# Performance work log

Measured on AMD Instinct MI355X. Metric: run time of the kernel, lower is better.

The kernel has to match this reference:

```python
import jax, jax.numpy as jnp
import numpy as np

N = 50000
E = 400000
T = 7
FEAT = 7
H = 64
OUT = 4
LN_EPS = 1e-5


def _w(key, shape, scale=0.1):
    return jax.random.normal(key, shape, jnp.float32) * scale


def setup_inputs() -> dict:
    key = jax.random.key(0)
    ks = list(jax.random.split(key, 16))
    p = {}
    p['x'] = jax.random.normal(ks[0], (N, T, FEAT), jnp.float32)
    p['edge_index'] = jax.random.randint(ks[1], (2, E), 0, N)
    p['edge_weight'] = jax.random.uniform(ks[2], (E,), jnp.float32)
    p['Wg1'] = _w(ks[3], (FEAT, H)); p['bg1'] = jnp.zeros((H,), jnp.float32)
    p['Wg2'] = _w(ks[4], (H, H));    p['bg2'] = jnp.zeros((H,), jnp.float32)
    p['ln_g'] = jnp.ones((H,), jnp.float32); p['ln_b'] = jnp.zeros((H,), jnp.float32)
    p['Wih0'] = _w(ks[5], (4 * H, H)); p['Whh0'] = _w(ks[6], (4 * H, H))
    p['bih0'] = jnp.zeros((4 * H,), jnp.float32); p['bhh0'] = jnp.zeros((4 * H,), jnp.float32)
    p['Wih1'] = _w(ks[7], (4 * H, H)); p['Whh1'] = _w(ks[8], (4 * H, H))
    p['bih1'] = jnp.zeros((4 * H,), jnp.float32); p['bhh1'] = jnp.zeros((4 * H,), jnp.float32)
    p['Wm1'] = _w(ks[9], (H, H // 2));  p['bm1'] = jnp.zeros((H // 2,), jnp.float32)
    p['Wm2'] = _w(ks[10], (H // 2, OUT)); p['bm2'] = jnp.zeros((OUT,), jnp.float32)
    p['Wd1'] = _w(ks[11], (H, H // 4)); p['bd1'] = jnp.zeros((H // 4,), jnp.float32)
    p['Wd2'] = _w(ks[12], (H // 4, OUT)); p['bd2'] = jnp.zeros((OUT,), jnp.float32)
    return p


def gcn_norm(edge_index, edge_weight, n):
    # PyG GCNConv default: add self-loops (weight 1), symmetric normalization
    loop = jnp.arange(n)
    src = jnp.concatenate([edge_index[0], loop])
    dst = jnp.concatenate([edge_index[1], loop])
    w = jnp.concatenate([edge_weight, jnp.ones((n,), edge_weight.dtype)])
    deg = jax.ops.segment_sum(w, dst, num_segments=n)
    dinv = jnp.where(deg > 0, jax.lax.rsqrt(deg), 0.0)
    return src, dst, dinv[src] * w * dinv[dst]


def gcn(h, W, b, src, dst, norm, n):
    h = h @ W                          # [N, H] linear transform first
    m = h[src] * norm[:, None]         # gather + edge scaling  [E', H]
    return jax.ops.segment_sum(m, dst, num_segments=n) + b


def layer_norm(h, g, b):
    mu = jnp.mean(h, -1, keepdims=True)
    v = jnp.mean((h - mu) ** 2, -1, keepdims=True)
    return (h - mu) * jax.lax.rsqrt(v + LN_EPS) * g + b


def lstm_layer(xs, Wih, Whh, bih, bhh):
    # xs: [N, T, H]; torch gate order i, f, g, o
    n = xs.shape[0]
    h0 = jnp.zeros((n, Whh.shape[1]), xs.dtype)
    def step(carry, xt):
        h, c = carry
        gates = xt @ Wih.T + h @ Whh.T + bih + bhh
        i, f, g, o = jnp.split(gates, 4, axis=-1)
        c = jax.nn.sigmoid(f) * c + jax.nn.sigmoid(i) * jnp.tanh(g)
        h = jax.nn.sigmoid(o) * jnp.tanh(c)
        return (h, c), h
    _, hs = jax.lax.scan(step, (h0, h0), jnp.swapaxes(xs, 0, 1))
    return jnp.swapaxes(hs, 0, 1)


def reference(x, edge_index, edge_weight, Wg1, bg1, Wg2, bg2, ln_g, ln_b,
              Wih0, Whh0, bih0, bhh0, Wih1, Whh1, bih1, bhh1,
              Wm1, bm1, Wm2, bm2, Wd1, bd1, Wd2, bd2):
    n = x.shape[0]
    src, dst, norm = gcn_norm(edge_index, edge_weight, n)
    outs = []
    for t in range(x.shape[1]):  # fixed small T=7 (lookback)
        h = gcn(x[:, t, :], Wg1, bg1, src, dst, norm, n)
        h = jax.nn.leaky_relu(h, 0.01)
        # dropout is identity in eval mode
        h = gcn(h, Wg2, bg2, src, dst, norm, n)
        h = jax.nn.leaky_relu(h, 0.01)
        h = layer_norm(h, ln_g, ln_b)
        outs.append(h)
    seq = jnp.stack(outs, axis=1)  # [N, T, H]
    seq = lstm_layer(seq, Wih0, Whh0, bih0, bhh0)
    seq = lstm_layer(seq, Wih1, Whh1, bih1, bhh1)
    f = seq[:, -1, :]
    magnitude = jax.nn.relu(jax.nn.leaky_relu(f @ Wm1 + bm1, 0.01) @ Wm2 + bm2) + 1e-4
    direction = jax.nn.relu(f @ Wd1 + bd1) @ Wd2 + bd2
    return (magnitude, direction)
```

## Files before the change

kernel.cpp:

```cpp
#include <hip/hip_runtime.h>
#include <stdint.h>

#define NN 50000
#define NP 50048
#define EE 400000
#define TT 7
#define LN_EPS 1e-5f
#define SIG_SC (-1.4426950408889634f)
#define TANH_SC (2.8853900817779268f)

typedef __attribute__((ext_vector_type(8))) short bf16x8;
typedef __attribute__((ext_vector_type(4))) float f32x4;

__device__ __forceinline__ float leaky01(float x){ return x > 0.f ? x : 0.01f*x; }
__device__ __forceinline__ float fastrcp(float x){ return __builtin_amdgcn_rcpf(x); }
__device__ __forceinline__ float exp2fast(float x){ return __builtin_amdgcn_exp2f(x); }
__device__ __forceinline__ unsigned bf16rne(float f){
  unsigned u = __float_as_uint(f);
  return (u + 0x7fffu + ((u>>16)&1u)) >> 16;
}
__device__ __forceinline__ float bfu(unsigned u){ return __uint_as_float(u<<16); }
__device__ __forceinline__ float bfhi(unsigned u){ return __uint_as_float(u & 0xffff0000u); }

__global__ __launch_bounds__(256) void k_prep_all(
    const float* __restrict__ Wih0, const float* __restrict__ Whh0,
    const float* __restrict__ Wih1, const float* __restrict__ Whh1,
    const float* __restrict__ Wg2,
    const float* __restrict__ bih0, const float* __restrict__ bhh0,
    const float* __restrict__ bih1, const float* __restrict__ bhh1,
    const float* __restrict__ Wm1, const float* __restrict__ Wd1,
    const float* __restrict__ x,
    uint4* __restrict__ WF, uint4* __restrict__ WG2F, uint4* __restrict__ WHF,
    float* __restrict__ BS,
    ushort* __restrict__ xb, float* __restrict__ deg, int* __restrict__ counts){
  int b = blockIdx.x, tid = threadIdx.x;
  if (b < 32){
    int idx = b*256 + tid;
    int L = idx >> 12;
    int r = idx & 4095;
    int lane = r & 63;
    int e = r >> 6;
    int which = e & 1;
    int cs = e >> 1;
    int s = cs & 1, ct = cs >> 1;
    int row = ct*16 + (lane & 15);
    float sc = ((row >> 6) == 2) ? TANH_SC : SIG_SC;
    int kb = s*32 + (lane >> 4)*8;
    const float* W = L ? (which ? Whh1 : Wih1) : (which ? Whh0 : Wih0);
    const float* p = W + row*64 + kb;
    uint4 v;
    v.x = bf16rne(sc*p[0]) | (bf16rne(sc*p[1])<<16);
    v.y = bf16rne(sc*p[2]) | (bf16rne(sc*p[3])<<16);
    v.z = bf16rne(sc*p[4]) | (bf16rne(sc*p[5])<<16);
    v.w = bf16rne(sc*p[6]) | (bf16rne(sc*p[7])<<16);
    WF[idx] = v;
  } else if (b < 34){
    int idx = (b-32)*256 + tid;
    int lane = idx & 63, e = idx >> 6;
    int s = e & 1, ct = e >> 1;
    int kb = s*32 + (lane>>4)*8;
    int c = ct*16 + (lane&15);
    uint4 v;
    v.x = bf16rne(Wg2[(kb+0)*64+c]) | (bf16rne(Wg2[(kb+1)*64+c])<<16);
    v.y = bf16rne(Wg2[(kb+2)*64+c]) | (bf16rne(Wg2[(kb+3)*64+c])<<16);
    v.z = bf16rne(Wg2[(kb+4)*64+c]) | (bf16rne(Wg2[(kb+5)*64+c])<<16);
    v.w = bf16rne(Wg2[(kb+6)*64+c]) | (bf16rne(Wg2[(kb+7)*64+c])<<16);
    WG2F[idx] = v;
  } else if (b < 36){
    int L = b - 34;
    float sc = ((tid >> 6) == 2) ? TANH_SC : SIG_SC;
    BS[L*256+tid] = sc * (L ? (bih1[tid]+bhh1[tid]) : (bih0[tid]+bhh0[tid]));
  } else if (b < 38){
    int idx = (b-36)*256 + tid;
    if (idx < 384){
      int lane = idx & 63, e = idx >> 6;
      int s = e & 1, ct = e >> 1;
      int kb = s*32 + (lane>>4)*8;
      int c = ct*16 + (lane&15);
      float w[8];
      #pragma unroll
      for (int j = 0; j < 8; ++j)
        w[j] = (c < 32) ? Wm1[(kb+j)*32 + c] : Wd1[(kb+j)*16 + (c-32)];
      uint4 v;
      v.x = bf16rne(w[0]) | (bf16rne(w[1])<<16);
      v.y = bf16rne(w[2]) | (bf16rne(w[3])<<16);
      v.z = bf16rne(w[4]) | (bf16rne(w[5])<<16);
      v.w = bf16rne(w[6]) | (bf16rne(w[7])<<16);
      WHF[idx] = v;
    }
  } else if (b < 234){
    int i = (b-38)*256 + tid;
    if (i < NN){ deg[i] = 1.0f; counts[i] = 0; }
  } else {
    int i = (b-234)*256 + tid;
    if (i < NN*49) xb[i] = (ushort)bf16rne(x[i]);
  }
}

__global__ void k_edge_count(const int* __restrict__ src, const int* __restrict__ dst,
                             const float* __restrict__ ew, float* deg, int* counts){
  int e = blockIdx.x*blockDim.x + threadIdx.x;
  if (e < EE){
    int d = dst[e];
    atomicAdd(&deg[d], ew[e]);
    atomicAdd(&counts[d], 1);
  }
}
__global__ __launch_bounds__(256) void k_scan_blk(const int* __restrict__ counts,
                                                  int* locincl, int* bsum, float* deg){
  int tid = threadIdx.x; int i = blockIdx.x*256 + tid;
  if (i < NN) deg[i] = rsqrtf(deg[i]);
  int v = (i < NN) ? counts[i] : 0;
  int lane = tid & 63;
  int val = v;
  #pragma unroll
  for (int off = 1; off < 64; off <<= 1){
    int u = __shfl_up(val, off, 64);
    if (lane >= off) val += u;
  }
  __shared__ int wsum[4];
  if (lane == 63) wsum[tid>>6] = val;
  __syncthreads();
  int w = tid >> 6, pre = 0;
  #pragma unroll
  for (int k = 0; k < 4; ++k) if (k < w) pre += wsum[k];
  int incl = val + pre;
  if (i < NN) locincl[i] = incl;
  if (tid == 255) bsum[blockIdx.x] = incl;
}
__global__ __launch_bounds__(256) void k_scan_top(const int* __restrict__ bsum, int* boff){
  int tid = threadIdx.x;
  int v = (tid < 196) ? bsum[tid] : 0;
  int lane = tid & 63;
  int val = v;
  #pragma unroll
  for (int off = 1; off < 64; off <<= 1){
    int u = __shfl_up(val, off, 64);
    if (lane >= off) val += u;
  }
  __shared__ int wsum[4];
  if (lane == 63) wsum[tid>>6] = val;
  __syncthreads();
  int w = tid >> 6, pre = 0;
  #pragma unroll
  for (int k = 0; k < 4; ++k) if (k < w) pre += wsum[k];
  if (tid < 196) boff[tid] = val + pre - v;
}
__global__ __launch_bounds__(256) void k_scan_fix(const int* __restrict__ locincl,
        const int* __restrict__ boff, const int* __restrict__ counts,
        int* rowptr, int* cursor){
  int i = blockIdx.x*256 + threadIdx.x;
  if (i < NN){
    int r = locincl[i] + boff[blockIdx.x];
    rowptr[i+1] = r;
    cursor[i] = r - counts[i];
  }
  if (i == 0) rowptr[0] = 0;
}
__global__ void k_scatter(const int* __restrict__ src, const int* __restrict__ dst,
                          const float* __restrict__ ew, const float* __restrict__ dinv,
                          int* cursor, uint2* e2){
  int e = blockIdx.x*blockDim.x + threadIdx.x;
  if (e < EE){
    int s = src[e], d = dst[e];
    float nv = dinv[s]*ew[e]*dinv[d];
    int slot = atomicAdd(&cursor[d], 1);
    e2[slot] = make_uint2((uint)s, __float_as_uint(nv));
  }
}

__global__ __launch_bounds__(256) void k_agg_x(const ushort* __restrict__ xb,
        const float* __restrict__ dinv, const int* __restrict__ rowptr,
        const uint2* __restrict__ e2, float* __restrict__ AX){
  int lane = threadIdx.x & 63, w = threadIdx.x >> 6;
  int i = blockIdx.x*4 + w;
  int beg = rowptr[i], end = rowptr[i+1];
  float di = dinv[i];
  float acc = 0.f;
  if (lane < 49) acc = di*di*bfu(xb[(size_t)i*49 + lane]);
  for (int s = beg; s < end; ++s){
    uint2 e = e2[s];
    int cs = (int)e.x; float wv = __uint_as_float(e.y);
    if (lane < 49) acc += wv * bfu(xb[(size_t)cs*49 + lane]);
  }
  if (lane < 49) AX[(size_t)i*49 + lane] = acc;
}
__global__ __launch_bounds__(256) void k_gcn2_mfma(const float* __restrict__ AX,
        const float* __restrict__ Wg1, const float* __restrict__ bg1,
        const uint4* __restrict__ WG2F, ushort* __restrict__ Z2p){
  __shared__ float sw1[448];
  __shared__ float sb1[64];
  __shared__ float sax[8*56];
  __shared__ __align__(16) ushort srb[64*68];
  int tid = threadIdx.x;
  int lane = tid & 63, w = tid >> 6;
  bf16x8 bw[4][2];
  #pragma unroll
  for (int ct = 0; ct < 4; ++ct)
    #pragma unroll
    for (int s = 0; s < 2; ++s){
      uint4 v = WG2F[(ct*2+s)*64 + lane];
      bw[ct][s] = *(bf16x8*)&v;
    }
  for (int i = tid; i < 448; i += 256) sw1[i] = Wg1[i];
  if (tid < 64) sb1[tid] = bg1[tid];
  int nbase = blockIdx.x*8;
  for (int i = tid; i < 448; i += 256){
    int n = i/56, c = i%56;
    sax[i] = (c < 49) ? AX[(size_t)(nbase+n)*49 + c] : 0.f;
  }
  __syncthreads();
  {
    int node = lane >> 3, t = lane & 7;
    float a[7];
    #pragma unroll
    for (int kk = 0; kk < 7; ++kk) a[kk] = sax[node*56 + t*7 + kk];
    ushort hv[16];
    #pragma unroll
    for (int j = 0; j < 16; ++j){
      int k = w*16 + j;
      float acc = sb1[k];
      #pragma unroll
      for (int kk = 0; kk < 7; ++kk) acc += a[kk]*sw1[kk*64+k];
      hv[j] = (ushort)bf16rne(leaky01(acc));
    }
    uint2* dst = (uint2*)&srb[lane*68 + w*16];
    #pragma unroll
    for (int q = 0; q < 4; ++q){
      uint2 v;
      v.x = (uint)hv[q*4+0] | ((uint)hv[q*4+1]<<16);
      v.y = (uint)hv[q*4+2] | ((uint)hv[q*4+3]<<16);
      dst[q] = v;
    }
  }
  __syncthreads();
  int col = lane & 15, quad = lane >> 4;
  bf16x8 afr[2];
  #pragma unroll
  for (int s = 0; s < 2; ++s){
    const ushort* pr = &srb[(w*16 + col)*68 + s*32 + quad*8];
    uint2 lo = *(const uint2*)pr;
    uint2 hi = *(const uint2*)(pr + 4);
    union { uint u[4]; bf16x8 b; } cv;
    cv.u[0]=lo.x; cv.u[1]=lo.y; cv.u[2]=hi.x; cv.u[3]=hi.y;
    afr[s] = cv.b;
  }
  f32x4 acc[4];
  #pragma unroll
  for (int ct = 0; ct < 4; ++ct) acc[ct] = (f32x4){0.f,0.f,0.f,0.f};
  #pragma unroll
  for (int ct = 0; ct < 4; ++ct)
    #pragma unroll
    for (int s = 0; s < 2; ++s)
      acc[ct] = __builtin_amdgcn_mfma_f32_16x16x32_bf16(afr[s], bw[ct][s], acc[ct], 0,0,0);
  int node = nbase + w*2 + (quad>>1);
  #pragma unroll
  for (int ct = 0; ct < 4; ++ct){
    uint2 v;
    v.x = bf16rne(acc[ct][0]) | (bf16rne(acc[ct][1])<<16);
    v.y = bf16rne(acc[ct][2]) | (bf16rne(acc[ct][3])<<16);
    size_t o = ((size_t)node*64 + ct*16 + col)*8 + (quad&1)*4;
    *(uint2*)(Z2p + o) = v;
  }
}
__global__ __launch_bounds__(256) void k_agg_ln_all(const ushort* __restrict__ Z2p,
        const float* __restrict__ dinv, const int* __restrict__ rowptr,
        const uint2* __restrict__ e2,
        const float* __restrict__ bg2, const float* __restrict__ lng,
        const float* __restrict__ lnb, ushort* __restrict__ XT){
  int lane = threadIdx.x & 63, w = threadIdx.x >> 6;
  int i = blockIdx.x*4 + w;
  int beg = rowptr[i], end = rowptr[i+1];
  float di = dinv[i];
  float swt = di*di;
  const uint4* zp = (const uint4*)Z2p;
  float acc[7];
  {
    uint4 v = zp[(size_t)i*64 + lane];
    acc[0] = swt*bfu(v.x); acc[1] = swt*bfhi(v.x);
    acc[2] = swt*bfu(v.y); acc[3] = swt*bfhi(v.y);
    acc[4] = swt*bfu(v.z); acc[5] = swt*bfhi(v.z);
    acc[6] = swt*bfu(v.w);
  }
  for (int s = beg; s < end; ++s){
    uint2 e = e2[s];
    int cs = (int)e.x; float wv = __uint_as_float(e.y);
    uint4 v = zp[(size_t)cs*64 + lane];
    acc[0] = fmaf(wv, bfu(v.x),  acc[0]);
    acc[1] = fmaf(wv, bfhi(v.x), acc[1]);
    acc[2] = fmaf(wv, bfu(v.y),  acc[2]);
    acc[3] = fmaf(wv, bfhi(v.y), acc[3]);
    acc[4] = fmaf(wv, bfu(v.z),  acc[4]);
    acc[5] = fmaf(wv, bfhi(v.z), acc[5]);
    acc[6] = fmaf(wv, bfu(v.w),  acc[6]);
  }
  float b2 = bg2[lane], gl = lng[lane], bl = lnb[lane];
  #pragma unroll
  for (int t = 0; t < 7; ++t){
    float a = leaky01(acc[t] + b2);
    float sum = a;
    #pragma unroll
    for (int off = 32; off >= 1; off >>= 1) sum += __shfl_xor(sum, off, 64);
    float mu = sum * (1.f/64.f);
    float d = a - mu;
    float vs = d*d;
    #pragma unroll
    for (int off = 32; off >= 1; off >>= 1) vs += __shfl_xor(vs, off, 64);
    float rs = rsqrtf(vs*(1.f/64.f) + LN_EPS);
    XT[(size_t)t*NP*64 + (size_t)i*64 + lane] = (ushort)bf16rne(d*rs*gl + bl);
  }
}

__global__ __launch_bounds__(256) void k_lstm_heads(const ushort* __restrict__ xin,
        const uint4* __restrict__ WF, const float* __restrict__ BS,
        const uint4* __restrict__ WHF,
        const float* __restrict__ bm1, const float* __restrict__ bd1,
        const float* __restrict__ Wm2, const float* __restrict__ bm2,
        const float* __restrict__ Wd2, const float* __restrict__ bd2,
        float* __restrict__ out){
  __shared__ __align__(16) ushort XL[7][16][72];
  int tid = threadIdx.x;
  int lane = tid & 63, cp = tid >> 6;
  int base = blockIdx.x*16;
  int col = lane & 15, quad = lane >> 4;
  bf16x8 hfr[2];
  hfr[0] = (bf16x8){0,0,0,0,0,0,0,0};
  hfr[1] = (bf16x8){0,0,0,0,0,0,0,0};

  for (int L = 0; L < 2; ++L){
    bf16x8 bwi[4][2], bwh[4][2];
    const uint4* wf = WF + L*4096;
    #pragma unroll
    for (int g = 0; g < 4; ++g){
      int ct = cp + 4*g;
      #pragma unroll
      for (int s = 0; s < 2; ++s){
        uint4 wi = wf[((ct*2+s)*2+0)*64 + lane];
        uint4 wh = wf[((ct*2+s)*2+1)*64 + lane];
        bwi[g][s] = *(bf16x8*)&wi;
        bwh[g][s] = *(bf16x8*)&wh;
      }
    }
    float bias[4];
    #pragma unroll
    for (int g = 0; g < 4; ++g) bias[g] = BS[L*256 + (cp + 4*g)*16 + col];
    f32x4 cst = (f32x4){0.f,0.f,0.f,0.f};
    if (L){
      hfr[0] = (bf16x8){0,0,0,0,0,0,0,0};
      hfr[1] = (bf16x8){0,0,0,0,0,0,0,0};
    }

    for (int t = 0; t < 7; ++t){
      bf16x8 ax[2];
      if (L == 0){
        #pragma unroll
        for (int s = 0; s < 2; ++s)
          ax[s] = *(const bf16x8*)(xin + (size_t)t*NP*64
                          + (size_t)(base + col)*64 + s*32 + quad*8);
      } else {
        #pragma unroll
        for (int s = 0; s < 2; ++s)
          ax[s] = *(const bf16x8*)&XL[t][col][s*32 + quad*8];
      }
      f32x4 acc[4];
      #pragma unroll
      for (int g = 0; g < 4; ++g){
        float b = bias[g];
        acc[g] = (f32x4){b,b,b,b};
      }
      #pragma unroll
      for (int g = 0; g < 4; ++g){
        #pragma unroll
        for (int s = 0; s < 2; ++s){
          acc[g] = __builtin_amdgcn_mfma_f32_16x16x32_bf16(ax[s], bwi[g][s], acc[g], 0,0,0);
          acc[g] = __builtin_amdgcn_mfma_f32_16x16x32_bf16(hfr[s], bwh[g][s], acc[g], 0,0,0);
        }
      }
      if (L) __syncthreads();
      #pragma unroll
      for (int r = 0; r < 4; ++r){
        float ig = fastrcp(1.f + exp2fast(acc[0][r]));
        float fg = fastrcp(1.f + exp2fast(acc[1][r]));
        float gg = fmaf(-2.f, fastrcp(1.f + exp2fast(acc[2][r])), 1.f);
        float og = fastrcp(1.f + exp2fast(acc[3][r]));
        float cn = fmaf(fg, cst[r], ig*gg);
        cst[r] = cn;
        float tc = fmaf(-2.f, fastrcp(1.f + exp2fast(TANH_SC*cn)), 1.f);
        XL[t][quad*4 + r][cp*16 + col] = (ushort)bf16rne(og*tc);
      }
      __syncthreads();
      hfr[0] = *(const bf16x8*)&XL[t][col][quad*8];
      hfr[1] = *(const bf16x8*)&XL[t][col][32 + quad*8];
    }
  }
  float* SH1 = (float*)&XL[0][0][0];
  if (cp < 3){
    uint4 w0 = WHF[(cp*2+0)*64 + lane];
    uint4 w1 = WHF[(cp*2+1)*64 + lane];
    float hb = (cp < 2) ? bm1[cp*16+col] : bd1[col];
    f32x4 hacc = (f32x4){hb,hb,hb,hb};
    hacc = __builtin_amdgcn_mfma_f32_16x16x32_bf16(hfr[0], *(bf16x8*)&w0, hacc, 0,0,0);
    hacc = __builtin_amdgcn_mfma_f32_16x16x32_bf16(hfr[1], *(bf16x8*)&w1, hacc, 0,0,0);
    #pragma unroll
    for (int r = 0; r < 4; ++r){
      float v = hacc[r];
      v = (cp < 2) ? leaky01(v) : fmaxf(v, 0.f);
      SH1[(quad*4 + r)*52 + cp*16 + col] = v;
    }
  }
  __syncthreads();
  int node = tid >> 4, sub = tid & 15;
  int gn = base + node;
  float m1a = SH1[node*52 + sub];
  float m1b = SH1[node*52 + 16 + sub];
  float d1v = SH1[node*52 + 32 + sub];
  float4 wa = *(const float4*)&Wm2[sub*4];
  float4 wb = *(const float4*)&Wm2[(sub+16)*4];
  float4 wc = *(const float4*)&Wd2[sub*4];
  float pm0 = m1a*wa.x + m1b*wb.x, pm1 = m1a*wa.y + m1b*wb.y;
  float pm2 = m1a*wa.z + m1b*wb.z, pm3 = m1a*wa.w + m1b*wb.w;
  float pd0 = d1v*wc.x, pd1 = d1v*wc.y, pd2 = d1v*wc.z, pd3 = d1v*wc.w;
  #pragma unroll
  for (int off = 1; off < 16; off <<= 1){
    pm0 += __shfl_xor(pm0, off, 16); pm1 += __shfl_xor(pm1, off, 16);
    pm2 += __shfl_xor(pm2, off, 16); pm3 += __shfl_xor(pm3, off, 16);
    pd0 += __shfl_xor(pd0, off, 16); pd1 += __shfl_xor(pd1, off, 16);
    pd2 += __shfl_xor(pd2, off, 16); pd3 += __shfl_xor(pd3, off, 16);
  }
  if (sub < 4 && gn < NN){
    float mo = (sub==0)?pm0:(sub==1)?pm1:(sub==2)?pm2:pm3;
    float dv = (sub==0)?pd0:(sub==1)?pd1:(sub==2)?pd2:pd3;
    mo += bm2[sub]; dv += bd2[sub];
    out[(size_t)gn*4 + sub] = fmaxf(mo, 0.f) + 1e-4f;
    out[(size_t)NN*4 + (size_t)gn*4 + sub] = dv;
  }
}

extern "C" void kernel_launch(void* const* d_in, const int* in_sizes, int n_in,
                              void* d_out, int out_size, void* d_ws, size_t ws_size,
                              hipStream_t stream){
  const float* x    = (const float*)d_in[0];
  const int*   eidx = (const int*)d_in[1];
  const float* ew   = (const float*)d_in[2];
  const float* Wg1  = (const float*)d_in[3];
  const float* bg1  = (const float*)d_in[4];
  const float* Wg2  = (const float*)d_in[5];
  const float* bg2  = (const float*)d_in[6];
  const float* lng  = (const float*)d_in[7];
  const float* lnb  = (const float*)d_in[8];
  const float* Wih0 = (const float*)d_in[9];
  const float* Whh0 = (const float*)d_in[10];
  const float* bih0 = (const float*)d_in[11];
  const float* bhh0 = (const float*)d_in[12];
  const float* Wih1 = (const float*)d_in[13];
  const float* Whh1 = (const float*)d_in[14];
  const float* bih1 = (const float*)d_in[15];
  const float* bhh1 = (const float*)d_in[16];
  const float* Wm1  = (const float*)d_in[17];
  const float* bm1  = (const float*)d_in[18];
  const float* Wm2  = (const float*)d_in[19];
  const float* bm2  = (const float*)d_in[20];
  const float* Wd1  = (const float*)d_in[21];
  const float* bd1  = (const float*)d_in[22];
  const float* Wd2  = (const float*)d_in[23];
  const float* bd2  = (const float*)d_in[24];
  const int* src = eidx;
  const int* dst = eidx + EE;
  float* out = (float*)d_out;

  char* p = (char*)d_ws;
  auto alloc = [&](size_t bytes)->char*{ char* r = p; p += (bytes + 255) & ~(size_t)255; return r; };
  float*  deg     = (float*)alloc((size_t)NN*4);
  int*    counts  = (int*)  alloc((size_t)NN*4);
  int*    rowptr  = (int*)  alloc((size_t)(NN+1)*4);
  int*    cursor  = (int*)  alloc((size_t)NN*4);
  int*    locincl = (int*)  alloc((size_t)NN*4);
  int*    bsum    = (int*)  alloc((size_t)256*4);
  int*    boff    = (int*)  alloc((size_t)256*4);
  uint2*  e2      = (uint2*)alloc((size_t)EE*8);
  uint4*  WF      = (uint4*)alloc((size_t)2*4096*16);
  uint4*  WG2F    = (uint4*)alloc((size_t)512*16);
  uint4*  WHF     = (uint4*)alloc((size_t)384*16);
  float*  BS      = (float*)alloc((size_t)2*256*4);
  ushort* xb      = (ushort*)alloc((size_t)NN*49*2);
  ushort* XT      = (ushort*)alloc((size_t)TT*NP*64*2);
  float*  AX      = (float*)alloc((size_t)NN*49*4);
  ushort* Z2p     = (ushort*)alloc((size_t)NN*64*8*2);

  int xblocks = (NN*49 + 255)/256;
  k_prep_all<<<234 + xblocks, 256, 0, stream>>>(Wih0, Whh0, Wih1, Whh1, Wg2,
      bih0, bhh0, bih1, bhh1, Wm1, Wd1, x, WF, WG2F, WHF, BS, xb, deg, counts);
  k_edge_count<<<(EE+255)/256, 256, 0, stream>>>(src, dst, ew, deg, counts);
  k_scan_blk<<<196, 256, 0, stream>>>(counts, locincl, bsum, deg);
  k_scan_top<<<1, 256, 0, stream>>>(bsum, boff);
  k_scan_fix<<<196, 256, 0, stream>>>(locincl, boff, counts, rowptr, cursor);
  k_scatter<<<(EE+255)/256, 256, 0, stream>>>(src, dst, ew, deg, cursor, e2);
  k_agg_x<<<NN/4, 256, 0, stream>>>(xb, deg, rowptr, e2, AX);
  k_gcn2_mfma<<<NN/8, 256, 0, stream>>>(AX, Wg1, bg1, WG2F, Z2p);
  k_agg_ln_all<<<NN/4, 256, 0, stream>>>(Z2p, deg, rowptr, e2, bg2, lng, lnb, XT);
  k_lstm_heads<<<NP/16, 256, 0, stream>>>(XT, WF, BS, WHF,
      bm1, bd1, Wm2, bm2, Wd2, bd2, out);
}
```

Measured before the change: 399.7 us.

## Fuse GCN aggregations into MFMA and LSTM kernels, dropping AX and XT buffers

Merges the first-layer feature aggregation into the GCN2 MFMA kernel, and the second aggregation plus LayerNorm into the LSTM/heads kernel, which writes normalized activations directly to shared memory. This removes two launches and the global round trips through the AX and XT intermediates. It also swaps MFMA operand order so each lane holds four consecutive hidden units, allowing vector bias loads and packed 8-byte LDS stores. In exchange the LSTM kernel gains a long irregular gather prologue per block, and each wave now aggregates several nodes serially, which may lower parallelism and latency hiding.

```diff
diff --git a/kernel.cpp b/kernel.cpp
--- a/kernel.cpp
+++ b/kernel.cpp
@@ -169,23 +169,9 @@
   }
 }
 
-__global__ __launch_bounds__(256) void k_agg_x(const ushort* __restrict__ xb,
+__global__ __launch_bounds__(256) void k_gcn_front(const ushort* __restrict__ xb,
         const float* __restrict__ dinv, const int* __restrict__ rowptr,
-        const uint2* __restrict__ e2, float* __restrict__ AX){
-  int lane = threadIdx.x & 63, w = threadIdx.x >> 6;
-  int i = blockIdx.x*4 + w;
-  int beg = rowptr[i], end = rowptr[i+1];
-  float di = dinv[i];
-  float acc = 0.f;
-  if (lane < 49) acc = di*di*bfu(xb[(size_t)i*49 + lane]);
-  for (int s = beg; s < end; ++s){
-    uint2 e = e2[s];
-    int cs = (int)e.x; float wv = __uint_as_float(e.y);
-    if (lane < 49) acc += wv * bfu(xb[(size_t)cs*49 + lane]);
-  }
-  if (lane < 49) AX[(size_t)i*49 + lane] = acc;
-}
-__global__ __launch_bounds__(256) void k_gcn2_mfma(const float* __restrict__ AX,
+        const uint2* __restrict__ e2,
         const float* __restrict__ Wg1, const float* __restrict__ bg1,
         const uint4* __restrict__ WG2F, ushort* __restrict__ Z2p){
   __shared__ float sw1[448];
@@ -205,9 +191,20 @@
   for (int i = tid; i < 448; i += 256) sw1[i] = Wg1[i];
   if (tid < 64) sb1[tid] = bg1[tid];
   int nbase = blockIdx.x*8;
-  for (int i = tid; i < 448; i += 256){
-    int n = i/56, c = i%56;
-    sax[i] = (c < 49) ? AX[(size_t)(nbase+n)*49 + c] : 0.f;
+  #pragma unroll
+  for (int j = 0; j < 2; ++j){
+    int n = w*2 + j;
+    int i = nbase + n;
+    int beg = rowptr[i], end = rowptr[i+1];
+    float di = dinv[i];
+    float acc = 0.f;
+    if (lane < 49) acc = di*di*bfu(xb[(size_t)i*49 + lane]);
+    for (int s = beg; s < end; ++s){
+      uint2 e = e2[s];
+      float wv = __uint_as_float(e.y);
+      if (lane < 49) acc += wv * bfu(xb[(size_t)e.x*49 + lane]);
+    }
+    if (lane < 56) sax[n*56 + lane] = (lane < 49) ? acc : 0.f;
   }
   __syncthreads();
   {
@@ -263,55 +260,12 @@
     *(uint2*)(Z2p + o) = v;
   }
 }
-__global__ __launch_bounds__(256) void k_agg_ln_all(const ushort* __restrict__ Z2p,
+
+__global__ __launch_bounds__(256) void k_gnn_lstm(const ushort* __restrict__ Z2p_,
         const float* __restrict__ dinv, const int* __restrict__ rowptr,
         const uint2* __restrict__ e2,
         const float* __restrict__ bg2, const float* __restrict__ lng,
-        const float* __restrict__ lnb, ushort* __restrict__ XT){
-  int lane = threadIdx.x & 63, w = threadIdx.x >> 6;
-  int i = blockIdx.x*4 + w;
-  int beg = rowptr[i], end = rowptr[i+1];
-  float di = dinv[i];
-  float swt = di*di;
-  const uint4* zp = (const uint4*)Z2p;
-  float acc[7];
-  {
-    uint4 v = zp[(size_t)i*64 + lane];
-    acc[0] = swt*bfu(v.x); acc[1] = swt*bfhi(v.x);
-    acc[2] = swt*bfu(v.y); acc[3] = swt*bfhi(v.y);
-    acc[4] = swt*bfu(v.z); acc[5] = swt*bfhi(v.z);
-    acc[6] = swt*bfu(v.w);
-  }
-  for (int s = beg; s < end; ++s){
-    uint2 e = e2[s];
-    int cs = (int)e.x; float wv = __uint_as_float(e.y);
-    uint4 v = zp[(size_t)cs*64 + lane];
-    acc[0] = fmaf(wv, bfu(v.x),  acc[0]);
-    acc[1] = fmaf(wv, bfhi(v.x), acc[1]);
-    acc[2] = fmaf(wv, bfu(v.y),  acc[2]);
-    acc[3] = fmaf(wv, bfhi(v.y), acc[3]);
-    acc[4] = fmaf(wv, bfu(v.z),  acc[4]);
-    acc[5] = fmaf(wv, bfhi(v.z), acc[5]);
-    acc[6] = fmaf(wv, bfu(v.w),  acc[6]);
-  }
-  float b2 = bg2[lane], gl = lng[lane], bl = lnb[lane];
-  #pragma unroll
-  for (int t = 0; t < 7; ++t){
-    float a = leaky01(acc[t] + b2);
-    float sum = a;
-    #pragma unroll
-    for (int off = 32; off >= 1; off >>= 1) sum += __shfl_xor(sum, off, 64);
-    float mu = sum * (1.f/64.f);
-    float d = a - mu;
-    float vs = d*d;
-    #pragma unroll
-    for (int off = 32; off >= 1; off >>= 1) vs += __shfl_xor(vs, off, 64);
-    float rs = rsqrtf(vs*(1.f/64.f) + LN_EPS);
-    XT[(size_t)t*NP*64 + (size_t)i*64 + lane] = (ushort)bf16rne(d*rs*gl + bl);
-  }
-}
-
-__global__ __launch_bounds__(256) void k_lstm_heads(const ushort* __restrict__ xin,
+        const float* __restrict__ lnb,
         const uint4* __restrict__ WF, const float* __restrict__ BS,
         const uint4* __restrict__ WHF,
         const float* __restrict__ bm1, const float* __restrict__ bd1,
@@ -323,10 +277,55 @@
   int lane = tid & 63, cp = tid >> 6;
   int base = blockIdx.x*16;
   int col = lane & 15, quad = lane >> 4;
+  const uint4* zp = (const uint4*)Z2p_;
+
+  {
+    float b2 = bg2[lane], gl = lng[lane], bl = lnb[lane];
+    for (int j = 0; j < 4; ++j){
+      int n = cp*4 + j;
+      int i = base + n;
+      float acc[7] = {0.f,0.f,0.f,0.f,0.f,0.f,0.f};
+      if (i < NN){
+        int beg = rowptr[i], end = rowptr[i+1];
+        float di = dinv[i];
+        float swt = di*di;
+        uint4 v = zp[(size_t)i*64 + lane];
+        acc[0] = swt*bfu(v.x); acc[1] = swt*bfhi(v.x);
+        acc[2] = swt*bfu(v.y); acc[3] = swt*bfhi(v.y);
+        acc[4] = swt*bfu(v.z); acc[5] = swt*bfhi(v.z);
+        acc[6] = swt*bfu(v.w);
+        for (int s = beg; s < end; ++s){
+          uint2 e = e2[s];
+          float wv = __uint_as_float(e.y);
+          uint4 vv = zp[(size_t)e.x*64 + lane];
+          acc[0] = fmaf(wv, bfu(vv.x),  acc[0]);
+          acc[1] = fmaf(wv, bfhi(vv.x), acc[1]);
+          acc[2] = fmaf(wv, bfu(vv.y),  acc[2]);
+          acc[3] = fmaf(wv, bfhi(vv.y), acc[3]);
+          acc[4] = fmaf(wv, bfu(vv.z),  acc[4]);
+          acc[5] = fmaf(wv, bfhi(vv.z), acc[5]);
+          acc[6] = fmaf(wv, bfu(vv.w),  acc[6]);
+        }
+      }
+      #pragma unroll
+      for (int t = 0; t < 7; ++t){
+        float a = leaky01(acc[t] + b2);
+        float sum = a;
+        #pragma unroll
+        for (int off = 32; off >= 1; off >>= 1) sum += __shfl_xor(sum, off, 64);
+        float mu = sum * (1.f/64.f);
+        float d = a - mu;
+        float vs = d*d;
+        #pragma unroll
+        for (int off = 32; off >= 1; off >>= 1) vs += __shfl_xor(vs, off, 64);
+        float rs = rsqrtf(vs*(1.f/64.f) + LN_EPS);
+        XL[t][n][lane] = (ushort)bf16rne(d*rs*gl + bl);
+      }
+    }
+  }
+  __syncthreads();
+
   bf16x8 hfr[2];
-  hfr[0] = (bf16x8){0,0,0,0,0,0,0,0};
-  hfr[1] = (bf16x8){0,0,0,0,0,0,0,0};
-
   for (int L = 0; L < 2; ++L){
     bf16x8 bwi[4][2], bwh[4][2];
     const uint4* wf = WF + L*4096;
@@ -341,42 +340,32 @@
         bwh[g][s] = *(bf16x8*)&wh;
       }
     }
-    float bias[4];
-    #pragma unroll
-    for (int g = 0; g < 4; ++g) bias[g] = BS[L*256 + (cp + 4*g)*16 + col];
+    f32x4 bias4[4];
+    #pragma unroll
+    for (int g = 0; g < 4; ++g)
+      bias4[g] = *(const f32x4*)&BS[L*256 + (cp + 4*g)*16 + quad*4];
     f32x4 cst = (f32x4){0.f,0.f,0.f,0.f};
-    if (L){
-      hfr[0] = (bf16x8){0,0,0,0,0,0,0,0};
-      hfr[1] = (bf16x8){0,0,0,0,0,0,0,0};
-    }
+    hfr[0] = (bf16x8){0,0,0,0,0,0,0,0};
+    hfr[1] = (bf16x8){0,0,0,0,0,0,0,0};
 
     for (int t = 0; t < 7; ++t){
       bf16x8 ax[2];
-      if (L == 0){
-        #pragma unroll
-        for (int s = 0; s < 2; ++s)
-          ax[s] = *(const bf16x8*)(xin + (size_t)t*NP*64
-                          + (size_t)(base + col)*64 + s*32 + quad*8);
-      } else {
-        #pragma unroll
-        for (int s = 0; s < 2; ++s)
-          ax[s] = *(const bf16x8*)&XL[t][col][s*32 + quad*8];
-      }
+      #pragma unroll
+      for (int s = 0; s < 2; ++s)
+        ax[s] = *(const bf16x8*)&XL[t][col][s*32 + quad*8];
       f32x4 acc[4];
       #pragma unroll
-      for (int g = 0; g < 4; ++g){
-        float b = bias[g];
-        acc[g] = (f32x4){b,b,b,b};
-      }
+      for (int g = 0; g < 4; ++g) acc[g] = bias4[g];
       #pragma unroll
       for (int g = 0; g < 4; ++g){
         #pragma unroll
         for (int s = 0; s < 2; ++s){
-          acc[g] = __builtin_amdgcn_mfma_f32_16x16x32_bf16(ax[s], bwi[g][s], acc[g], 0,0,0);
-          acc[g] = __builtin_amdgcn_mfma_f32_16x16x32_bf16(hfr[s], bwh[g][s], acc[g], 0,0,0);
+          acc[g] = __builtin_amdgcn_mfma_f32_16x16x32_bf16(bwi[g][s], ax[s], acc[g], 0,0,0);
+          acc[g] = __builtin_amdgcn_mfma_f32_16x16x32_bf16(bwh[g][s], hfr[s], acc[g], 0,0,0);
         }
       }
-      if (L) __syncthreads();
+      __syncthreads();
+      ushort hv[4];
       #pragma unroll
       for (int r = 0; r < 4; ++r){
         float ig = fastrcp(1.f + exp2fast(acc[0][r]));
@@ -386,8 +375,12 @@
         float cn = fmaf(fg, cst[r], ig*gg);
         cst[r] = cn;
         float tc = fmaf(-2.f, fastrcp(1.f + exp2fast(TANH_SC*cn)), 1.f);
-        XL[t][quad*4 + r][cp*16 + col] = (ushort)bf16rne(og*tc);
+        hv[r] = (ushort)bf16rne(og*tc);
       }
+      uint2 hw;
+      hw.x = (uint)hv[0] | ((uint)hv[1]<<16);
+      hw.y = (uint)hv[2] | ((uint)hv[3]<<16);
+      *(uint2*)&XL[t][col][cp*16 + quad*4] = hw;
       __syncthreads();
       hfr[0] = *(const bf16x8*)&XL[t][col][quad*8];
       hfr[1] = *(const bf16x8*)&XL[t][col][32 + quad*8];
@@ -397,16 +390,18 @@
   if (cp < 3){
     uint4 w0 = WHF[(cp*2+0)*64 + lane];
     uint4 w1 = WHF[(cp*2+1)*64 + lane];
-    float hb = (cp < 2) ? bm1[cp*16+col] : bd1[col];
-    f32x4 hacc = (f32x4){hb,hb,hb,hb};
-    hacc = __builtin_amdgcn_mfma_f32_16x16x32_bf16(hfr[0], *(bf16x8*)&w0, hacc, 0,0,0);
-    hacc = __builtin_amdgcn_mfma_f32_16x16x32_bf16(hfr[1], *(bf16x8*)&w1, hacc, 0,0,0);
+    f32x4 hacc = (f32x4){0.f,0.f,0.f,0.f};
+    hacc = __builtin_amdgcn_mfma_f32_16x16x32_bf16(*(bf16x8*)&w0, hfr[0], hacc, 0,0,0);
+    hacc = __builtin_amdgcn_mfma_f32_16x16x32_bf16(*(bf16x8*)&w1, hfr[1], hacc, 0,0,0);
+    float sv[4];
     #pragma unroll
     for (int r = 0; r < 4; ++r){
-      float v = hacc[r];
-      v = (cp < 2) ? leaky01(v) : fmaxf(v, 0.f);
-      SH1[(quad*4 + r)*52 + cp*16 + col] = v;
-    }
+      int c = cp*16 + quad*4 + r;
+      float b = (cp < 2) ? bm1[c] : bd1[c - 32];
+      float v = hacc[r] + b;
+      sv[r] = (cp < 2) ? leaky01(v) : fmaxf(v, 0.f);
+    }
+    *(float4*)&SH1[col*52 + cp*16 + quad*4] = make_float4(sv[0], sv[1], sv[2], sv[3]);
   }
   __syncthreads();
   int node = tid >> 4, sub = tid & 15;
@@ -483,8 +478,6 @@
   uint4*  WHF     = (uint4*)alloc((size_t)384*16);
   float*  BS      = (float*)alloc((size_t)2*256*4);
   ushort* xb      = (ushort*)alloc((size_t)NN*49*2);
-  ushort* XT      = (ushort*)alloc((size_t)TT*NP*64*2);
-  float*  AX      = (float*)alloc((size_t)NN*49*4);
   ushort* Z2p     = (ushort*)alloc((size_t)NN*64*8*2);
 
   int xblocks = (NN*49 + 255)/256;
@@ -495,9 +488,7 @@
   k_scan_top<<<1, 256, 0, stream>>>(bsum, boff);
   k_scan_fix<<<196, 256, 0, stream>>>(locincl, boff, counts, rowptr, cursor);
   k_scatter<<<(EE+255)/256, 256, 0, stream>>>(src, dst, ew, deg, cursor, e2);
-  k_agg_x<<<NN/4, 256, 0, stream>>>(xb, deg, rowptr, e2, AX);
-  k_gcn2_mfma<<<NN/8, 256, 0, stream>>>(AX, Wg1, bg1, WG2F, Z2p);
-  k_agg_ln_all<<<NN/4, 256, 0, stream>>>(Z2p, deg, rowptr, e2, bg2, lng, lnb, XT);
-  k_lstm_heads<<<NP/16, 256, 0, stream>>>(XT, WF, BS, WHF,
-      bm1, bd1, Wm2, bm2, Wd2, bd2, out);
-}
+  k_gcn_front<<<NN/8, 256, 0, stream>>>(xb, deg, rowptr, e2, Wg1, bg1, WG2F, Z2p);
+  k_gnn_lstm<<<NP/16, 256, 0, stream>>>(Z2p, deg, rowptr, e2, bg2, lng, lnb,
+      WF, BS, WHF, bm1, bd1, Wm2, bm2, Wd2, bd2, out);
+}
```

Result: slower. 474.7 us (+18.7%).
